# Kernel tuning notes

Measured on AMD Instinct MI355X. Metric: run time of the kernel, lower is better.

The kernel has to match this reference:

```python
import jax, jax.numpy as jnp
import numpy as np

D_MODEL = 1024
N_HEADS = 16
D_K = D_MODEL // N_HEADS


def setup_inputs() -> dict:
    key = jax.random.key(0)
    ks = jax.random.split(key, 5)
    scale = 1.0 / np.sqrt(D_MODEL)
    x = jax.random.normal(ks[0], (4, 2048, D_MODEL), dtype=jnp.float32)
    W_Q = jax.random.uniform(ks[1], (D_MODEL, D_MODEL), jnp.float32, -scale, scale)
    W_K = jax.random.uniform(ks[2], (D_MODEL, D_MODEL), jnp.float32, -scale, scale)
    W_V = jax.random.uniform(ks[3], (D_MODEL, D_MODEL), jnp.float32, -scale, scale)
    W_O = jax.random.uniform(ks[4], (D_MODEL, D_MODEL), jnp.float32, -scale, scale)
    return {"x": x, "W_Q": W_Q, "W_K": W_K, "W_V": W_V, "W_O": W_O}


def reference(x, W_Q, W_K, W_V, W_O):
    B, S, _ = x.shape
    # nn.Linear(y) = y @ W.T ; weights stored (out, in)
    def heads(W):
        return jnp.einsum('bsd,ed->bse', x, W).reshape(B, S, N_HEADS, D_K).transpose(0, 2, 1, 3)
    Q, K, V = heads(W_Q), heads(W_K), heads(W_V)  # [B,H,S,Dk]
    scores = jnp.einsum('bhqd,bhkd->bhqk', Q, K) / np.sqrt(D_K)
    causal = jnp.tril(jnp.ones((S, S), dtype=bool))
    scores = jnp.where(causal[None, None], scores, -jnp.inf)
    attn = jax.nn.softmax(scores, axis=-1)  # [B,H,S,S]
    out = jnp.einsum('bhqk,bhkd->bhqd', attn, V)
    out = out.transpose(0, 2, 1, 3).reshape(B, S, D_MODEL)
    return jnp.einsum('bsd,ed->bse', out, W_O)
```

## Files before the change

### kernel.cpp

```cpp
#include <hip/hip_runtime.h>
#include <hip/hip_bf16.h>
#include <stdint.h>

#define D_MODEL 1024
#define NHEADS  16
#define DKH     64
#define BATCH   4
#define SEQ     2048
#define NTOK    (BATCH * SEQ)

typedef unsigned short u16;
using bf16x8 = __attribute__((ext_vector_type(8))) short;
using f32x4  = __attribute__((ext_vector_type(4))) float;
using f32x16 = __attribute__((ext_vector_type(16))) float;
using u32x2  = __attribute__((ext_vector_type(2))) unsigned int;

#define GLD16(g, l)                                                            \
  __builtin_amdgcn_global_load_lds(                                            \
      (const __attribute__((address_space(1))) void*)(g),                      \
      (__attribute__((address_space(3))) void*)(l), 16, 0, 0)

__device__ inline u16 f2bf(float f) {
  __hip_bfloat16 h = __float2bfloat16(f);
  return __builtin_bit_cast(u16, h);
}

__device__ inline float fexp2(float x) { return __builtin_amdgcn_exp2f(x); }

__device__ inline unsigned cvtpk(float lo, float hi) {
  unsigned r;
  asm("v_cvt_pk_bf16_f32 %0, %1, %2" : "=v"(r) : "v"(lo), "v"(hi));
  return r;
}

template <int B>
__device__ inline bf16x8 make_pfrag(const f32x16& sv) {
  unsigned x1 = cvtpk(sv[B + 0], sv[B + 1]);
  unsigned y1 = cvtpk(sv[B + 4], sv[B + 5]);
  unsigned x2 = cvtpk(sv[B + 2], sv[B + 3]);
  unsigned y2 = cvtpk(sv[B + 6], sv[B + 7]);
  u32x2 s1 = __builtin_amdgcn_permlane32_swap(x1, y1, false, false);
  u32x2 s2 = __builtin_amdgcn_permlane32_swap(x2, y2, false, false);
  union { unsigned u[4]; bf16x8 v; } r;
  r.u[0] = s1[0]; r.u[1] = s2[0]; r.u[2] = s1[1]; r.u[3] = s2[1];
  return r.v;
}

__global__ __launch_bounds__(256) void cvt_all(const float* __restrict__ x,
                                               const float* __restrict__ wq,
                                               const float* __restrict__ wk,
                                               const float* __restrict__ wv,
                                               const float* __restrict__ wo,
                                               u16* xb, u16* wqb, u16* wkb, u16* wvb, u16* wob) {
  const int XC = NTOK * D_MODEL / 4;
  const int WC = D_MODEL * D_MODEL / 4;
  const int total = XC + 4 * WC;
  for (int i = blockIdx.x * 256 + threadIdx.x; i < total; i += gridDim.x * 256) {
    const float4* s; ushort4* d; int j;
    if (i < XC)              { s = (const float4*)x;  d = (ushort4*)xb;  j = i; }
    else if (i < XC + WC)    { s = (const float4*)wq; d = (ushort4*)wqb; j = i - XC; }
    else if (i < XC + 2*WC)  { s = (const float4*)wk; d = (ushort4*)wkb; j = i - XC - WC; }
    else if (i < XC + 3*WC)  { s = (const float4*)wv; d = (ushort4*)wvb; j = i - XC - 2*WC; }
    else                     { s = (const float4*)wo; d = (ushort4*)wob; j = i - XC - 3*WC; }
    float4 v = s[j];
    d[j] = make_ushort4(f2bf(v.x), f2bf(v.y), f2bf(v.z), f2bf(v.w));
  }
}

__global__ __launch_bounds__(256) void gemm_qkv(const u16* __restrict__ A,
                                                const u16* __restrict__ Bq,
                                                const u16* __restrict__ Bk,
                                                const u16* __restrict__ Bv,
                                                u16* __restrict__ Qo,
                                                u16* __restrict__ Ko,
                                                u16* __restrict__ Vo) {
  __shared__ u16 As[2][128 * 64];
  __shared__ u16 Bs[2][128 * 64];
  const int h = blockIdx.x;
  const int L = (h & 7) * 192 + (h >> 3);
  const int z = L / 512;
  const int rr = L % 512;
  const int bM = (rr >> 3) * 128;
  const int bN = (rr & 7) * 128;
  const u16* __restrict__ Bp = z == 0 ? Bq : (z == 1 ? Bk : Bv);
  const int t = threadIdx.x, lane = t & 63, wave = t >> 6;
  const int wr = wave >> 1, wc = wave & 1;
  const int frow = lane & 15, g = lane >> 4;

  auto stage = [&](int buf, int k0) {
#pragma unroll
    for (int p = 0; p < 4; ++p) {
      int chunk = p * 256 + t;
      int r = chunk >> 3, cc = chunk & 7;
      int cs = cc ^ (r & 7);
      GLD16(A + (size_t)(bM + r) * D_MODEL + k0 + cs * 8, &As[buf][(size_t)(p * 256 + (t & ~63)) * 8]);
      GLD16(Bp + (size_t)(bN + r) * D_MODEL + k0 + cs * 8, &Bs[buf][(size_t)(p * 256 + (t & ~63)) * 8]);
    }
  };

  f32x4 acc[4][4] = {};
  stage(0, 0);
  __syncthreads();

  int cur = 0;
  for (int k0 = 0; k0 < D_MODEL; k0 += 64) {
    if (k0 + 64 < D_MODEL) stage(cur ^ 1, k0 + 64);

    bf16x8 a[2][4], b[2][4];
#pragma unroll
    for (int kk = 0; kk < 2; ++kk) {
#pragma unroll
      for (int m = 0; m < 4; ++m)
        a[kk][m] = *(const bf16x8*)&As[cur][(wr * 64 + m * 16 + frow) * 64 +
                                           (((kk * 4 + g) ^ (frow & 7)) * 8)];
#pragma unroll
      for (int n = 0; n < 4; ++n)
        b[kk][n] = *(const bf16x8*)&Bs[cur][(wc * 64 + n * 16 + frow) * 64 +
                                           (((kk * 4 + g) ^ (frow & 7)) * 8)];
    }
#pragma unroll
    for (int kk = 0; kk < 2; ++kk)
#pragma unroll
      for (int m = 0; m < 4; ++m)
#pragma unroll
        for (int n = 0; n < 4; ++n)
          acc[m][n] = __builtin_amdgcn_mfma_f32_16x16x32_bf16(a[kk][m], b[kk][n], acc[m][n], 0, 0, 0);

    __syncthreads();
    cur ^= 1;
  }

  const int r0 = bM + wr * 64 + (lane >> 4) * 4;
  const int c0 = bN + wc * 64 + (lane & 15);
  if (z == 2) {
#pragma unroll
    for (int m = 0; m < 4; ++m)
#pragma unroll
      for (int n = 0; n < 4; ++n) {
        int r = r0 + m * 16;
        int cc = c0 + n * 16;
        size_t off = ((size_t)(r >> 11) * D_MODEL + cc) * SEQ + (r & (SEQ - 1));
        *(ushort4*)(Vo + off) = make_ushort4(f2bf(acc[m][n][0]), f2bf(acc[m][n][1]),
                                             f2bf(acc[m][n][2]), f2bf(acc[m][n][3]));
      }
  } else {
    u16* C = z ? Ko : Qo;
    const float sc = z ? 1.0f : 0.18033688f;
#pragma unroll
    for (int m = 0; m < 4; ++m)
#pragma unroll
      for (int n = 0; n < 4; ++n)
#pragma unroll
        for (int j = 0; j < 4; ++j)
          C[(size_t)(r0 + m * 16 + j) * D_MODEL + (c0 + n * 16)] = f2bf(acc[m][n][j] * sc);
  }
}

__global__ __launch_bounds__(256) void gemm_out(const u16* __restrict__ A,
                                                const u16* __restrict__ B,
                                                float* __restrict__ C) {
  __shared__ u16 As[2][128 * 64];
  __shared__ u16 Bs[2][128 * 64];
  const int h = blockIdx.x;
  const int L = (h & 7) * 64 + (h >> 3);
  const int bM = (L >> 3) * 128;
  const int bN = (L & 7) * 128;
  const int t = threadIdx.x, lane = t & 63, wave = t >> 6;
  const int wr = wave >> 1, wc = wave & 1;
  const int frow = lane & 15, g = lane >> 4;

  auto stage = [&](int buf, int k0) {
#pragma unroll
    for (int p = 0; p < 4; ++p) {
      int chunk = p * 256 + t;
      int r = chunk >> 3, cc = chunk & 7;
      int cs = cc ^ (r & 7);
      GLD16(A + (size_t)(bM + r) * D_MODEL + k0 + cs * 8, &As[buf][(size_t)(p * 256 + (t & ~63)) * 8]);
      GLD16(B + (size_t)(bN + r) * D_MODEL + k0 + cs * 8, &Bs[buf][(size_t)(p * 256 + (t & ~63)) * 8]);
    }
  };

  f32x4 acc[4][4] = {};
  stage(0, 0);
  __syncthreads();

  int cur = 0;
  for (int k0 = 0; k0 < D_MODEL; k0 += 64) {
    if (k0 + 64 < D_MODEL) stage(cur ^ 1, k0 + 64);

    bf16x8 a[2][4], b[2][4];
#pragma unroll
    for (int kk = 0; kk < 2; ++kk) {
#pragma unroll
      for (int m = 0; m < 4; ++m)
        a[kk][m] = *(const bf16x8*)&As[cur][(wr * 64 + m * 16 + frow) * 64 +
                                           (((kk * 4 + g) ^ (frow & 7)) * 8)];
#pragma unroll
      for (int n = 0; n < 4; ++n)
        b[kk][n] = *(const bf16x8*)&Bs[cur][(wc * 64 + n * 16 + frow) * 64 +
                                           (((kk * 4 + g) ^ (frow & 7)) * 8)];
    }
#pragma unroll
    for (int kk = 0; kk < 2; ++kk)
#pragma unroll
      for (int m = 0; m < 4; ++m)
#pragma unroll
        for (int n = 0; n < 4; ++n)
          acc[m][n] = __builtin_amdgcn_mfma_f32_16x16x32_bf16(a[kk][m], b[kk][n], acc[m][n], 0, 0, 0);

    __syncthreads();
    cur ^= 1;
  }

  const int r0 = bM + wr * 64 + (lane >> 4) * 4;
  const int c0 = bN + wc * 64 + (lane & 15);
#pragma unroll
  for (int m = 0; m < 4; ++m)
#pragma unroll
    for (int n = 0; n < 4; ++n)
#pragma unroll
      for (int j = 0; j < 4; ++j)
        C[(size_t)(r0 + m * 16 + j) * D_MODEL + (c0 + n * 16)] = acc[m][n][j];
}

__global__ __launch_bounds__(256) void attn_fwd(const u16* __restrict__ Q,
                                                const u16* __restrict__ K,
                                                const u16* __restrict__ Vt,
                                                u16* __restrict__ O) {
  __shared__ u16 Kl[2][64 * 64];
  __shared__ u16 Vl[2][64 * 64];
  const int t = threadIdx.x, lane = t & 63, wave = t >> 6;
  const int q = lane & 31, hi = lane >> 5;
  const int bh = blockIdx.x & 63;
  const int qtile = 15 - (blockIdx.x >> 6);
  const int q0 = qtile * 128;
  const size_t rowbase = (size_t)(bh >> 4) * SEQ;
  const int hcol = (bh & 15) * DKH;
  const size_t vbase = (size_t)bh * DKH;
  const int qw = q0 + wave * 32;
  const int nit = qtile * 2 + 2;

  auto stage = [&](int buf, int kv0) {
#pragma unroll
    for (int pp = 0; pp < 2; ++pp) {
      int chunk = pp * 256 + t;
      int r = chunk >> 3, cc = chunk & 7;
      int cs = cc ^ (r & 7);
      GLD16(K + (rowbase + kv0 + r) * D_MODEL + hcol + cs * 8,
            &Kl[buf][(size_t)(pp * 256 + (t & ~63)) * 8]);
      GLD16(Vt + (vbase + r) * SEQ + kv0 + cs * 8,
            &Vl[buf][(size_t)(pp * 256 + (t & ~63)) * 8]);
    }
  };

  stage(0, 0);

  bf16x8 qf[4];
#pragma unroll
  for (int w = 0; w < 4; ++w)
    qf[w] = *(const bf16x8*)&Q[(rowbase + qw + q) * D_MODEL + hcol + w * 16 + hi * 8];

  f32x16 ot0 = {}, ot1 = {};
  float mstate = -__builtin_inff();
  float lstate = 0.f;

  __syncthreads();
  int cur = 0;
  for (int it = 0; it < nit; ++it) {
    const int kv0 = it * 64;
    if (it + 1 < nit) stage(cur ^ 1, kv0 + 64);

    if (kv0 <= qw + 31) {
      f32x16 s0 = {}, s1 = {};
      __builtin_amdgcn_s_setprio(1);
#pragma unroll
      for (int w = 0; w < 4; ++w) {
        const int rk0 = q, rk1 = 32 + q;
        bf16x8 k0 = *(const bf16x8*)&Kl[cur][rk0 * 64 + (((2 * w + hi) ^ (rk0 & 7)) * 8)];
        bf16x8 k1 = *(const bf16x8*)&Kl[cur][rk1 * 64 + (((2 * w + hi) ^ (rk0 & 7)) * 8)];
        s0 = __builtin_amdgcn_mfma_f32_32x32x16_bf16(k0, qf[w], s0, 0, 0, 0);
        s1 = __builtin_amdgcn_mfma_f32_32x32x16_bf16(k1, qf[w], s1, 0, 0, 0);
      }
      __builtin_amdgcn_s_setprio(0);

      const int qg = qw + q;
      if (kv0 + 63 > qw) {
#pragma unroll
        for (int r = 0; r < 16; ++r) {
          const int crow = (r & 3) + 8 * (r >> 2) + 4 * hi;
          if (kv0 + crow > qg) s0[r] = -__builtin_inff();
          if (kv0 + 32 + crow > qg) s1[r] = -__builtin_inff();
        }
      }

      float mx[16];
#pragma unroll
      for (int r = 0; r < 16; ++r) mx[r] = fmaxf(s0[r], s1[r]);
#pragma unroll
      for (int w2 = 8; w2 > 0; w2 >>= 1)
#pragma unroll
        for (int r = 0; r < w2; ++r) mx[r] = fmaxf(mx[r], mx[r + w2]);
      float pmax = fmaxf(mx[0], __shfl_xor(mx[0], 32));

      if (__any(pmax > mstate + 11.5416f)) {
        float mnew = fmaxf(mstate, pmax);
        float al = fexp2(mstate - mnew);
        mstate = mnew;
        lstate *= al;
#pragma unroll
        for (int r = 0; r < 16; ++r) { ot0[r] *= al; ot1[r] *= al; }
      }
      const float mm = mstate;

      float sm[16];
#pragma unroll
      for (int r = 0; r < 16; ++r) {
        s0[r] = fexp2(s0[r] - mm);
        s1[r] = fexp2(s1[r] - mm);
        sm[r] = s0[r] + s1[r];
      }
#pragma unroll
      for (int w2 = 8; w2 > 0; w2 >>= 1)
#pragma unroll
        for (int r = 0; r < w2; ++r) sm[r] += sm[r + w2];
      lstate += sm[0] + __shfl_xor(sm[0], 32);

      bf16x8 pb0 = make_pfrag<0>(s0);
      bf16x8 pb1 = make_pfrag<8>(s0);
      bf16x8 pb2 = make_pfrag<0>(s1);
      bf16x8 pb3 = make_pfrag<8>(s1);

      __builtin_amdgcn_s_setprio(1);
#define PV_STEP(KB, PB)                                                                   \
      {                                                                                   \
        bf16x8 v0 = *(const bf16x8*)&Vl[cur][q * 64 + (((2 * (KB) + hi) ^ (q & 7)) * 8)]; \
        bf16x8 v1 = *(const bf16x8*)&Vl[cur][(32 + q) * 64 + (((2 * (KB) + hi) ^ (q & 7)) * 8)]; \
        ot0 = __builtin_amdgcn_mfma_f32_32x32x16_bf16(v0, PB, ot0, 0, 0, 0);              \
        ot1 = __builtin_amdgcn_mfma_f32_32x32x16_bf16(v1, PB, ot1, 0, 0, 0);              \
      }
      PV_STEP(0, pb0)
      PV_STEP(1, pb1)
      PV_STEP(2, pb2)
      PV_STEP(3, pb3)
#undef PV_STEP
      __builtin_amdgcn_s_setprio(0);
    }
    __syncthreads();
    cur ^= 1;
  }

  const float inv = 1.0f / lstate;
  u16* orow = &O[(rowbase + qw + q) * D_MODEL + hcol];
#pragma unroll
  for (int g2 = 0; g2 < 4; ++g2) {
    ushort4 a4 = make_ushort4(f2bf(ot0[4 * g2 + 0] * inv), f2bf(ot0[4 * g2 + 1] * inv),
                              f2bf(ot0[4 * g2 + 2] * inv), f2bf(ot0[4 * g2 + 3] * inv));
    *(ushort4*)&orow[8 * g2 + 4 * hi] = a4;
    ushort4 b4 = make_ushort4(f2bf(ot1[4 * g2 + 0] * inv), f2bf(ot1[4 * g2 + 1] * inv),
                              f2bf(ot1[4 * g2 + 2] * inv), f2bf(ot1[4 * g2 + 3] * inv));
    *(ushort4*)&orow[32 + 8 * g2 + 4 * hi] = b4;
  }
}

extern "C" void kernel_launch(void* const* d_in, const int* in_sizes, int n_in,
                              void* d_out, int out_size, void* d_ws, size_t ws_size,
                              hipStream_t stream) {
  const float* x  = (const float*)d_in[0];
  const float* Wq = (const float*)d_in[1];
  const float* Wk = (const float*)d_in[2];
  const float* Wv = (const float*)d_in[3];
  const float* Wo = (const float*)d_in[4];
  float* out = (float*)d_out;

  u16* ws  = (u16*)d_ws;
  u16* xb  = ws;
  u16* wqb = xb + (size_t)NTOK * D_MODEL;
  u16* wkb = wqb + (size_t)D_MODEL * D_MODEL;
  u16* wvb = wkb + (size_t)D_MODEL * D_MODEL;
  u16* wob = wvb + (size_t)D_MODEL * D_MODEL;
  u16* Qb  = wob + (size_t)D_MODEL * D_MODEL;
  u16* Kb  = Qb + (size_t)NTOK * D_MODEL;
  u16* Vb  = Kb + (size_t)NTOK * D_MODEL;
  u16* Ob  = xb;

  cvt_all<<<2048, 256, 0, stream>>>(x, Wq, Wk, Wv, Wo, xb, wqb, wkb, wvb, wob);

  gemm_qkv<<<1536, 256, 0, stream>>>(xb, wqb, wkb, wvb, Qb, Kb, Vb);

  attn_fwd<<<dim3(16 * 64), 256, 0, stream>>>(Qb, Kb, Vb, Ob);

  gemm_out<<<512, 256, 0, stream>>>(Ob, wob, out);
}
```

Measured before the change: 165.6 us.

## Single-buffer LDS in projection GEMMs and use max3 tree in softmax row max

Both projection GEMM kernels drop the double-buffered LDS prefetch and switch to a single buffer loaded and synchronised each K step. This halves shared memory per block, which may allow more resident blocks, but global loads no longer overlap with MFMA work. The attention kernel also reorganises its row-max reduction into three-operand max calls so the compiler can emit v_max3 instructions.

```diff
diff --git a/kernel.cpp b/kernel.cpp
--- a/kernel.cpp
+++ b/kernel.cpp
@@ -26,6 +26,8 @@
 }
 
 __device__ inline float fexp2(float x) { return __builtin_amdgcn_exp2f(x); }
+
+__device__ inline float fmax3(float a, float b, float c) { return fmaxf(fmaxf(a, b), c); }
 
 __device__ inline unsigned cvtpk(float lo, float hi) {
   unsigned r;
@@ -74,8 +76,8 @@
                                                 u16* __restrict__ Qo,
                                                 u16* __restrict__ Ko,
                                                 u16* __restrict__ Vo) {
-  __shared__ u16 As[2][128 * 64];
-  __shared__ u16 Bs[2][128 * 64];
+  __shared__ u16 As[128 * 64];
+  __shared__ u16 Bs[128 * 64];
   const int h = blockIdx.x;
   const int L = (h & 7) * 192 + (h >> 3);
   const int z = L / 512;
@@ -87,36 +89,31 @@
   const int wr = wave >> 1, wc = wave & 1;
   const int frow = lane & 15, g = lane >> 4;
 
-  auto stage = [&](int buf, int k0) {
+  f32x4 acc[4][4] = {};
+
+  for (int k0 = 0; k0 < D_MODEL; k0 += 64) {
+    __syncthreads();
 #pragma unroll
     for (int p = 0; p < 4; ++p) {
       int chunk = p * 256 + t;
       int r = chunk >> 3, cc = chunk & 7;
       int cs = cc ^ (r & 7);
-      GLD16(A + (size_t)(bM + r) * D_MODEL + k0 + cs * 8, &As[buf][(size_t)(p * 256 + (t & ~63)) * 8]);
-      GLD16(Bp + (size_t)(bN + r) * D_MODEL + k0 + cs * 8, &Bs[buf][(size_t)(p * 256 + (t & ~63)) * 8]);
-    }
-  };
-
-  f32x4 acc[4][4] = {};
-  stage(0, 0);
-  __syncthreads();
-
-  int cur = 0;
-  for (int k0 = 0; k0 < D_MODEL; k0 += 64) {
-    if (k0 + 64 < D_MODEL) stage(cur ^ 1, k0 + 64);
+      GLD16(A + (size_t)(bM + r) * D_MODEL + k0 + cs * 8, As + (size_t)(p * 256 + (t & ~63)) * 8);
+      GLD16(Bp + (size_t)(bN + r) * D_MODEL + k0 + cs * 8, Bs + (size_t)(p * 256 + (t & ~63)) * 8);
+    }
+    __syncthreads();
 
     bf16x8 a[2][4], b[2][4];
 #pragma unroll
     for (int kk = 0; kk < 2; ++kk) {
 #pragma unroll
       for (int m = 0; m < 4; ++m)
-        a[kk][m] = *(const bf16x8*)&As[cur][(wr * 64 + m * 16 + frow) * 64 +
-                                           (((kk * 4 + g) ^ (frow & 7)) * 8)];
+        a[kk][m] = *(const bf16x8*)&As[(wr * 64 + m * 16 + frow) * 64 +
+                                      (((kk * 4 + g) ^ (frow & 7)) * 8)];
 #pragma unroll
       for (int n = 0; n < 4; ++n)
-        b[kk][n] = *(const bf16x8*)&Bs[cur][(wc * 64 + n * 16 + frow) * 64 +
-                                           (((kk * 4 + g) ^ (frow & 7)) * 8)];
+        b[kk][n] = *(const bf16x8*)&Bs[(wc * 64 + n * 16 + frow) * 64 +
+                                      (((kk * 4 + g) ^ (frow & 7)) * 8)];
     }
 #pragma unroll
     for (int kk = 0; kk < 2; ++kk)
@@ -125,9 +122,6 @@
 #pragma unroll
         for (int n = 0; n < 4; ++n)
           acc[m][n] = __builtin_amdgcn_mfma_f32_16x16x32_bf16(a[kk][m], b[kk][n], acc[m][n], 0, 0, 0);
-
-    __syncthreads();
-    cur ^= 1;
   }
 
   const int r0 = bM + wr * 64 + (lane >> 4) * 4;
@@ -159,8 +153,8 @@
 __global__ __launch_bounds__(256) void gemm_out(const u16* __restrict__ A,
                                                 const u16* __restrict__ B,
                                                 float* __restrict__ C) {
-  __shared__ u16 As[2][128 * 64];
-  __shared__ u16 Bs[2][128 * 64];
+  __shared__ u16 As[128 * 64];
+  __shared__ u16 Bs[128 * 64];
   const int h = blockIdx.x;
   const int L = (h & 7) * 64 + (h >> 3);
   const int bM = (L >> 3) * 128;
@@ -169,36 +163,31 @@
   const int wr = wave >> 1, wc = wave & 1;
   const int frow = lane & 15, g = lane >> 4;
 
-  auto stage = [&](int buf, int k0) {
+  f32x4 acc[4][4] = {};
+
+  for (int k0 = 0; k0 < D_MODEL; k0 += 64) {
+    __syncthreads();
 #pragma unroll
     for (int p = 0; p < 4; ++p) {
       int chunk = p * 256 + t;
       int r = chunk >> 3, cc = chunk & 7;
       int cs = cc ^ (r & 7);
-      GLD16(A + (size_t)(bM + r) * D_MODEL + k0 + cs * 8, &As[buf][(size_t)(p * 256 + (t & ~63)) * 8]);
-      GLD16(B + (size_t)(bN + r) * D_MODEL + k0 + cs * 8, &Bs[buf][(size_t)(p * 256 + (t & ~63)) * 8]);
-    }
-  };
-
-  f32x4 acc[4][4] = {};
-  stage(0, 0);
-  __syncthreads();
-
-  int cur = 0;
-  for (int k0 = 0; k0 < D_MODEL; k0 += 64) {
-    if (k0 + 64 < D_MODEL) stage(cur ^ 1, k0 + 64);
+      GLD16(A + (size_t)(bM + r) * D_MODEL + k0 + cs * 8, As + (size_t)(p * 256 + (t & ~63)) * 8);
+      GLD16(B + (size_t)(bN + r) * D_MODEL + k0 + cs * 8, Bs + (size_t)(p * 256 + (t & ~63)) * 8);
+    }
+    __syncthreads();
 
     bf16x8 a[2][4], b[2][4];
 #pragma unroll
     for (int kk = 0; kk < 2; ++kk) {
 #pragma unroll
       for (int m = 0; m < 4; ++m)
-        a[kk][m] = *(const bf16x8*)&As[cur][(wr * 64 + m * 16 + frow) * 64 +
-                                           (((kk * 4 + g) ^ (frow & 7)) * 8)];
+        a[kk][m] = *(const bf16x8*)&As[(wr * 64 + m * 16 + frow) * 64 +
+                                      (((kk * 4 + g) ^ (frow & 7)) * 8)];
 #pragma unroll
       for (int n = 0; n < 4; ++n)
-        b[kk][n] = *(const bf16x8*)&Bs[cur][(wc * 64 + n * 16 + frow) * 64 +
-                                           (((kk * 4 + g) ^ (frow & 7)) * 8)];
+        b[kk][n] = *(const bf16x8*)&Bs[(wc * 64 + n * 16 + frow) * 64 +
+                                      (((kk * 4 + g) ^ (frow & 7)) * 8)];
     }
 #pragma unroll
     for (int kk = 0; kk < 2; ++kk)
@@ -207,9 +196,6 @@
 #pragma unroll
         for (int n = 0; n < 4; ++n)
           acc[m][n] = __builtin_amdgcn_mfma_f32_16x16x32_bf16(a[kk][m], b[kk][n], acc[m][n], 0, 0, 0);
-
-    __syncthreads();
-    cur ^= 1;
   }
 
   const int r0 = bM + wr * 64 + (lane >> 4) * 4;
@@ -296,11 +282,15 @@
       float mx[16];
 #pragma unroll
       for (int r = 0; r < 16; ++r) mx[r] = fmaxf(s0[r], s1[r]);
-#pragma unroll
-      for (int w2 = 8; w2 > 0; w2 >>= 1)
-#pragma unroll
-        for (int r = 0; r < w2; ++r) mx[r] = fmaxf(mx[r], mx[r + w2]);
-      float pmax = fmaxf(mx[0], __shfl_xor(mx[0], 32));
+      float a0 = fmax3(mx[0], mx[1], mx[2]);
+      float a1 = fmax3(mx[3], mx[4], mx[5]);
+      float a2 = fmax3(mx[6], mx[7], mx[8]);
+      float a3 = fmax3(mx[9], mx[10], mx[11]);
+      float a4 = fmax3(mx[12], mx[13], mx[14]);
+      float b0 = fmax3(a0, a1, mx[15]);
+      float b1 = fmax3(a2, a3, a4);
+      float pmax = fmaxf(b0, b1);
+      pmax = fmaxf(pmax, __shfl_xor(pmax, 32));
 
       if (__any(pmax > mstate + 11.5416f)) {
         float mnew = fmaxf(mstate, pmax);
```

New measurement: 172.5 us. 1.04x slower.
